# Kernel optimization log

Measured on AMD Instinct MI355X. Metric: run time of the kernel, lower is better.

Reference implementation:

```python
import jax, jax.numpy as jnp
import numpy as np

B, H, W, C = 8, 256, 256, 32
WIN = 8
HEADS = 2
DH = C // HEADS          # 16
HIDDEN = 128             # mlp_ratio * C
N = WIN * WIN            # 64 tokens per window


def _rel_index(win):
    # standard Swin relative position index, computed once (static int constant)
    coords = np.stack(np.meshgrid(np.arange(win), np.arange(win), indexing='ij'))  # [2,w,w]
    coords = coords.reshape(2, -1)                                                  # [2,N]
    rel = (coords[:, :, None] - coords[:, None, :]).transpose(1, 2, 0)              # [N,N,2]
    rel[:, :, 0] += win - 1
    rel[:, :, 1] += win - 1
    rel[:, :, 0] *= 2 * win - 1
    return jnp.asarray(rel.sum(-1))                                                 # [N,N]

REL_IDX = _rel_index(WIN)


def setup_inputs() -> dict:
    key = jax.random.key(0)
    ks = jax.random.split(key, 10)
    rn = lambda k, s: jax.random.normal(k, s, jnp.float32) * 0.02
    return {
        'x': jax.random.normal(ks[0], (B, H * W, C), jnp.float32),
        'norm1_g': jnp.ones((C,), jnp.float32), 'norm1_b': jnp.zeros((C,), jnp.float32),
        'wq': rn(ks[1], (C, C)), 'bq': jnp.zeros((C,), jnp.float32),
        'wkv': rn(ks[2], (C, 2 * C)), 'bkv': jnp.zeros((2 * C,), jnp.float32),
        'wo': rn(ks[3], (C, C)), 'bo': jnp.zeros((C,), jnp.float32),
        'rel_bias': rn(ks[4], ((2 * WIN - 1) ** 2, HEADS)),
        'norm2_g': jnp.ones((C,), jnp.float32), 'norm2_b': jnp.zeros((C,), jnp.float32),
        'w1': rn(ks[5], (C, HIDDEN)), 'b1': jnp.zeros((HIDDEN,), jnp.float32),
        'dw': rn(ks[6], (HIDDEN, 1, 3, 3)), 'dwb': jnp.zeros((HIDDEN,), jnp.float32),
        'w2': rn(ks[7], (HIDDEN, C)), 'b2': jnp.zeros((C,), jnp.float32),
    }


def _ln(x, g, b):
    mu = x.mean(-1, keepdims=True)
    var = x.var(-1, keepdims=True)
    return (x - mu) / jnp.sqrt(var + 1e-5) * g + b


def _gelu(x):
    return jax.nn.gelu(x, approximate=False)  # torch nn.GELU is exact erf


def reference(x, norm1_g, norm1_b, wq, bq, wkv, bkv, wo, bo, rel_bias,
              norm2_g, norm2_b, w1, b1, dw, dwb, w2, b2):
    shortcut = x                                              # [B, HW, C]
    xn = _ln(x, norm1_g, norm1_b).reshape(B, H, W, C)
    # window partition -> [B*nW, N, C]
    xw = (xn.reshape(B, H // WIN, WIN, W // WIN, WIN, C)
            .transpose(0, 1, 3, 2, 4, 5)
            .reshape(-1, N, C))
    # linear qkv projection
    q = (xw @ wq + bq).reshape(-1, N, HEADS, DH).transpose(0, 2, 1, 3)      # [B_,h,N,d]
    kv = (xw @ wkv + bkv).reshape(-1, N, 2, HEADS, DH).transpose(2, 0, 3, 1, 4)
    k, v = kv[0], kv[1]
    scale = DH ** -0.5
    attn = jnp.einsum('bhnd,bhmd->bhnm', q * scale, k)                      # [B_,h,N,N]
    bias = rel_bias[REL_IDX].transpose(2, 0, 1)                             # [h,N,N]
    attn = jax.nn.softmax(attn + bias[None], axis=-1)
    out = jnp.einsum('bhnm,bhmd->bhnd', attn, v).transpose(0, 2, 1, 3).reshape(-1, N, C)
    out = out @ wo + bo
    # window reverse -> [B, HW, C]
    out = (out.reshape(B, H // WIN, W // WIN, WIN, WIN, C)
              .transpose(0, 1, 3, 2, 4, 5)
              .reshape(B, H * W, C))
    x = shortcut + out
    # LeFF: linear -> dwconv3x3 over full HxW map -> linear
    y = _ln(x, norm2_g, norm2_b)
    y = _gelu(y @ w1 + b1)                                                  # [B,HW,HIDDEN]
    y = y.reshape(B, H, W, HIDDEN).transpose(0, 3, 1, 2)                    # NCHW
    y = jax.lax.conv_general_dilated(
        y, dw, window_strides=(1, 1), padding='SAME',
        dimension_numbers=('NCHW', 'OIHW', 'NCHW'), feature_group_count=HIDDEN)
    y = _gelu(y + dwb[None, :, None, None])
    y = y.transpose(0, 2, 3, 1).reshape(B, H * W, HIDDEN)
    y = y @ w2 + b2
    return x + y
```

## Files before the change

### kernel.cpp

```cpp
#include <hip/hip_runtime.h>
#include <hip/hip_bf16.h>
#include <math.h>

#define IMG   256
#define HWTOK 65536
#define CH    32

typedef __attribute__((ext_vector_type(8))) _Float16 half8v;
typedef __attribute__((ext_vector_type(2))) _Float16 half2v;
typedef __attribute__((ext_vector_type(4))) float floatx4;

__device__ __forceinline__ unsigned short f2h(float f) {
    _Float16 h = (_Float16)f;
    return __builtin_bit_cast(unsigned short, h);
}
__device__ __forceinline__ half2v pkrtz(float a, float b) {
    return __builtin_bit_cast(half2v, __builtin_amdgcn_cvt_pkrtz(a, b));
}
__device__ __forceinline__ unsigned packh2(float a, float b) {
    return __builtin_bit_cast(unsigned, __builtin_amdgcn_cvt_pkrtz(a, b));
}

__device__ __forceinline__ half2v gelu2v(half2v v) {
    const half2v hi = (half2v)(_Float16)( 2.0f);
    const half2v lo = (half2v)(_Float16)(-2.0f);
    const half2v vc = __builtin_elementwise_min(__builtin_elementwise_max(v, lo), hi);
    const half2v s  = vc * vc;
    half2v p = s * (half2v)(_Float16)(-1.18726e-3f) + (half2v)(_Float16)(9.97356e-3f);
    p = s * p + (half2v)(_Float16)(-6.64904e-2f);
    p = s * p + (half2v)(_Float16)( 3.989423e-1f);
    return v * (vc * p + (half2v)(_Float16)(0.5f));
}

__global__ __launch_bounds__(256) void prep_kernel(
    const float* __restrict__ w1, const float* __restrict__ w2,
    const float* __restrict__ wq, const float* __restrict__ wkv,
    const float* __restrict__ wo, const float* __restrict__ dw,
    const float* __restrict__ dwb, const float* __restrict__ relb,
    unsigned short* __restrict__ w1p, unsigned short* __restrict__ w2p,
    unsigned short* __restrict__ wqp, unsigned short* __restrict__ wkp,
    unsigned short* __restrict__ wvp, unsigned short* __restrict__ wop,
    unsigned short* __restrict__ dwp, unsigned short* __restrict__ dwbp,
    float* __restrict__ biasf)
{
    const float LOG2E = 1.4426950408889634f;
    const float QSC   = 0.25f * LOG2E;
    const int bid = blockIdx.x, tid = threadIdx.x;

    if (bid < 16) {
        const int t = bid * 256 + tid;
        const int row = t >> 5, k = t & 31;
        const int bl = row >> 5, wi = row & 31;
        const int j = bl * 32 + ((wi & 15) << 1) + (wi >> 4);
        w1p[t] = f2h(w1[k * 128 + j]);
        const int n = t >> 7, kk = t & 127;
        w2p[t] = f2h(w2[kk * 32 + n]);
    } else if (bid < 20) {
        const int u = (bid - 16) * 256 + tid;
        const int h = u >> 9, rem = u & 511;
        const int col = rem >> 5, k = rem & 31;
        wqp[u] = f2h(wq [k * 32 + h * 16 + col] * QSC);
        wkp[u] = f2h(wkv[k * 64 + h * 16 + col]);
        wvp[u] = f2h(wkv[k * 64 + 32 + h * 16 + col]);
        const int n = u >> 5, kk2 = u & 31;
        wop[u] = f2h(wo[kk2 * 32 + n]);
    } else if (bid < 28) {
        const int g = (bid - 20) * 256 + tid;
        const int h = g >> 10, nt = (g >> 8) & 3, mt = (g >> 6) & 3, l = g & 63;
        const int q = nt * 16 + (l & 15);
        const int mb = mt * 16 + (l >> 4) * 4;
        const int qy = q >> 3, qx = q & 7;
        #pragma unroll
        for (int r = 0; r < 4; ++r) {
            const int m = mb + r;
            const int my = m >> 3, mx = m & 7;
            const int idx = (qy - my + 7) * 15 + (qx - mx + 7);
            biasf[g * 4 + r] = relb[idx * 2 + h] * LOG2E;
        }
    } else {
        for (int e = tid; e < 1280; e += 256) {
            if (e < 1152) dwp[e] = f2h(dw[(e & 127) * 9 + (e >> 7)]);
            else          dwbp[e - 1152] = f2h(dwb[e - 1152]);
        }
    }
}

__global__ __launch_bounds__(128) void attn_kernel(
    const float* __restrict__ x,
    const float* __restrict__ n1g, const float* __restrict__ n1b,
    const float* __restrict__ bq,  const float* __restrict__ bkv,
    const float* __restrict__ bo,
    const unsigned short* __restrict__ wqp,
    const unsigned short* __restrict__ wkp,
    const unsigned short* __restrict__ wvp,
    const unsigned short* __restrict__ wop,
    const float4* __restrict__ biasf4,
    float* __restrict__ x1)
{
    struct Win {
        union {
            unsigned short xn[64][40];
            unsigned short P[2][64][72];
            unsigned short O[64][40];
        } u;
        unsigned short Q[64][40];
        unsigned short K[64][48];
        unsigned short VT[2][16][72];
    };
    __shared__ Win S;
    __shared__ float denom[2][64];

    const int tid = threadIdx.x;
    const int h   = tid >> 6;
    const int l   = tid & 63;
    const int lm  = l & 15, lq = l >> 4;

    const int win = blockIdx.x;
    const int b   = win >> 10;
    const int wh  = (win >> 5) & 31, ww = win & 31;
    const size_t wbase = ((size_t)b * HWTOK + (wh * 8) * IMG + ww * 8) * CH;

    const float LOG2E = 1.4426950408889634f;
    const float QSC   = 0.25f * LOG2E;

    const half8v bwq  = *(const half8v*)&wqp[h * 512 + lm * 32 + lq * 8];
    const half8v bwk  = *(const half8v*)&wkp[h * 512 + lm * 32 + lq * 8];
    const half8v bwv  = *(const half8v*)&wvp[h * 512 + lm * 32 + lq * 8];
    const half8v bwo0 = *(const half8v*)&wop[lm * 32 + lq * 8];
    const half8v bwo1 = *(const half8v*)&wop[(16 + lm) * 32 + lq * 8];

    {
        const int tok = tid >> 1, half = tid & 1;
        const size_t sbase = wbase
            + (size_t)((tok >> 3) * IMG + (tok & 7)) * CH + half * 16;
        const float4* xp = (const float4*)(x + sbase);
        float v[16];
        float s = 0.f;
        #pragma unroll
        for (int i = 0; i < 4; ++i) {
            const float4 t = xp[i];
            v[i*4+0]=t.x; v[i*4+1]=t.y; v[i*4+2]=t.z; v[i*4+3]=t.w;
            s += t.x + t.y + t.z + t.w;
        }
        const float mu = (s + __shfl_xor(s, 1)) * (1.f / 32.f);
        float qq = 0.f;
        #pragma unroll
        for (int c = 0; c < 16; ++c) { const float d = v[c] - mu; qq += d * d; }
        const float var = qq + __shfl_xor(qq, 1);
        const float inv = rsqrtf(var * (1.f / 32.f) + 1e-5f);
        unsigned pk[8];
        #pragma unroll
        for (int j = 0; j < 8; ++j) {
            const int c = half * 16 + 2 * j;
            pk[j] = packh2((v[2*j]   - mu) * inv * n1g[c]   + n1b[c],
                           (v[2*j+1] - mu) * inv * n1g[c+1] + n1b[c+1]);
        }
        uint4* dst = (uint4*)&S.u.xn[tok][half * 16];
        dst[0] = *(uint4*)&pk[0];
        dst[1] = *(uint4*)&pk[4];
        const uint4 z = {0u, 0u, 0u, 0u};
        *(uint4*)&S.K[tok][16 + half * 8] = z;
    }
    __syncthreads();

    const float bqv = bq[h*16 + lm] * QSC;
    const float bkv_ = bkv[h*16 + lm];
    const float bvv = bkv[32 + h*16 + lm];
    const floatx4 cq = {bqv, bqv, bqv, bqv};
    const floatx4 ck = {bkv_, bkv_, bkv_, bkv_};
    const floatx4 cv = {bvv, bvv, bvv, bvv};
    const floatx4 zero = {0.f, 0.f, 0.f, 0.f};

    #pragma unroll
    for (int mt = 0; mt < 4; ++mt) {
        const half8v a = *(const half8v*)&S.u.xn[mt*16 + lm][lq*8];
        const floatx4 dq = __builtin_amdgcn_mfma_f32_16x16x32_f16(a, bwq, cq, 0,0,0);
        const floatx4 dk = __builtin_amdgcn_mfma_f32_16x16x32_f16(a, bwk, ck, 0,0,0);
        const floatx4 dv = __builtin_amdgcn_mfma_f32_16x16x32_f16(a, bwv, cv, 0,0,0);
        const int r0 = mt*16 + lq*4;
        #pragma unroll
        for (int r = 0; r < 4; ++r) {
            S.Q[r0 + r][h*16 + lm] = f2h(dq[r]);
            S.K[r0 + r][h*32 + lm] = f2h(dk[r]);
        }
        uint2 vv;
        vv.x = packh2(dv[0], dv[1]);
        vv.y = packh2(dv[2], dv[3]);
        *(uint2*)&S.VT[h][lm][r0] = vv;
    }
    __syncthreads();

    half8v ak[4], bqf[4];
    #pragma unroll
    for (int mt = 0; mt < 4; ++mt)
        ak[mt] = *(const half8v*)&S.K[mt*16 + lm][h*16 + lq*8];
    #pragma unroll
    for (int nt = 0; nt < 4; ++nt)
        bqf[nt] = *(const half8v*)&S.Q[nt*16 + lm][lq*8];

    #pragma unroll
    for (int nt = 0; nt < 4; ++nt) {
        float sum = 0.f;
        #pragma unroll
        for (int mt = 0; mt < 4; ++mt) {
            const float4 cb = biasf4[(h*16 + nt*4 + mt) * 64 + l];
            const floatx4 C = {cb.x, cb.y, cb.z, cb.w};
            const floatx4 d = __builtin_amdgcn_mfma_f32_16x16x32_f16(ak[mt], bqf[nt], C, 0,0,0);
            const float e0 = exp2f(d[0]);
            const float e1 = exp2f(d[1]);
            const float e2 = exp2f(d[2]);
            const float e3 = exp2f(d[3]);
            sum += (e0 + e1) + (e2 + e3);
            uint2 pw;
            pw.x = packh2(e0, e1);
            pw.y = packh2(e2, e3);
            *(uint2*)&S.u.P[h][nt*16 + lm][mt*16 + lq*4] = pw;
        }
        sum += __shfl_xor(sum, 16);
        sum += __shfl_xor(sum, 32);
        if (l < 16) denom[h][nt*16 + l] = __frcp_rn(sum);
    }

    const half8v bva = *(const half8v*)&S.VT[h][lm][lq*8];
    const half8v bvb = *(const half8v*)&S.VT[h][lm][32 + lq*8];
    float oreg[16];
    #pragma unroll
    for (int mt = 0; mt < 4; ++mt) {
        const half8v ap0 = *(const half8v*)&S.u.P[h][mt*16 + lm][lq*8];
        const half8v ap1 = *(const half8v*)&S.u.P[h][mt*16 + lm][32 + lq*8];
        floatx4 ov = __builtin_amdgcn_mfma_f32_16x16x32_f16(ap0, bva, zero, 0,0,0);
        ov         = __builtin_amdgcn_mfma_f32_16x16x32_f16(ap1, bvb, ov,   0,0,0);
        const float4 dn = *(const float4*)&denom[h][mt*16 + lq*4];
        oreg[mt*4+0] = ov[0] * dn.x;
        oreg[mt*4+1] = ov[1] * dn.y;
        oreg[mt*4+2] = ov[2] * dn.z;
        oreg[mt*4+3] = ov[3] * dn.w;
    }
    __syncthreads();

    #pragma unroll
    for (int mt = 0; mt < 4; ++mt)
        #pragma unroll
        for (int r = 0; r < 4; ++r)
            S.u.O[mt*16 + lq*4 + r][h*16 + lm] = f2h(oreg[mt*4 + r]);
    __syncthreads();

    const float bo0 = bo[lm], bo1 = bo[16 + lm];
    const floatx4 co0 = {bo0, bo0, bo0, bo0};
    const floatx4 co1 = {bo1, bo1, bo1, bo1};
    #pragma unroll
    for (int mi = 0; mi < 2; ++mi) {
        const int mt = 2*h + mi;
        const half8v aO = *(const half8v*)&S.u.O[mt*16 + lm][lq*8];
        const floatx4 d0 = __builtin_amdgcn_mfma_f32_16x16x32_f16(aO, bwo0, co0, 0,0,0);
        const floatx4 d1 = __builtin_amdgcn_mfma_f32_16x16x32_f16(aO, bwo1, co1, 0,0,0);
        #pragma unroll
        for (int r = 0; r < 4; ++r) {
            const int t = mt*16 + lq*4 + r;
            const size_t g = wbase + (size_t)((t >> 3) * IMG + (t & 7)) * CH;
            x1[g + lm]      = x[g + lm]      + d0[r];
            x1[g + 16 + lm] = x[g + 16 + lm] + d1[r];
        }
    }
}

__global__ __launch_bounds__(256, 3) void leff_kernel_gw(
    const float* __restrict__ x1,
    const float* __restrict__ n2g, const float* __restrict__ n2b,
    const float* __restrict__ b1,  const float* __restrict__ b2,
    const unsigned short* __restrict__ w1p,
    const unsigned short* __restrict__ w2p,
    const unsigned short* __restrict__ dwp,
    const unsigned short* __restrict__ dwbp,
    float* __restrict__ out)
{
    __shared__ __align__(16) unsigned short xnA[112][40];
    union HG {
        unsigned short hid[100][128];
        unsigned short glA[64][132];
    };
    __shared__ __align__(16) HG hg;

    const int blk = blockIdx.x;
    const int b = blk >> 10, tyb = (blk >> 5) & 31, txb = blk & 31;
    const int y0 = tyb * 8, x0 = txb * 8;
    const int tid = threadIdx.x;
    const int wv = tid >> 6;
    const int l  = tid & 63;
    const int lm = l & 15;
    const int lq = l >> 4;
    const bool edge = (tyb == 0) | (tyb == 31) | (txb == 0) | (txb == 31);

    const half8v bf0 = *(const half8v*)&w1p[(wv * 32 + lm) * 32 + lq * 8];
    const half8v bf1 = *(const half8v*)&w1p[(wv * 32 + 16 + lm) * 32 + lq * 8];

    if (tid < 200) {
        const int px = tid >> 1, half = tid & 1;
        const int hy = px / 10, hx = px % 10;
        const int iy = y0 + hy - 1, ix = x0 + hx - 1;
        const bool inb = (iy >= 0 && iy < IMG && ix >= 0 && ix < IMG);
        unsigned int pk[8];
        if (inb) {
            const size_t base = ((size_t)b * HWTOK + iy * IMG + ix) * CH + half * 16;
            const float4* xp = (const float4*)(x1 + base);
            float v[16];
            float s = 0.f;
            #pragma unroll
            for (int i = 0; i < 4; ++i) {
                const float4 t = xp[i];
                v[i*4+0]=t.x; v[i*4+1]=t.y; v[i*4+2]=t.z; v[i*4+3]=t.w;
                s += t.x + t.y + t.z + t.w;
            }
            const float mu = (s + __shfl_xor(s, 1)) * (1.f / 32.f);
            float q = 0.f;
            #pragma unroll
            for (int c = 0; c < 16; ++c) { const float d = v[c]-mu; q += d*d; }
            const float var = q + __shfl_xor(q, 1);
            const float inv = rsqrtf(var * (1.f/32.f) + 1e-5f);
            #pragma unroll
            for (int j = 0; j < 8; ++j) {
                const int c = half*16 + 2*j;
                pk[j] = packh2((v[2*j]   - mu) * inv * n2g[c]   + n2b[c],
                               (v[2*j+1] - mu) * inv * n2g[c+1] + n2b[c+1]);
            }
        } else {
            #pragma unroll
            for (int j = 0; j < 8; ++j) pk[j] = 0u;
        }
        uint4* dst = (uint4*)&xnA[px][half * 16];
        dst[0] = *(uint4*)&pk[0];
        dst[1] = *(uint4*)&pk[4];
    } else if (tid < 248) {
        const int t2 = tid - 200;
        const uint4 z = {0u,0u,0u,0u};
        *(uint4*)&xnA[100 + (t2 >> 2)][(t2 & 3) * 8] = z;
    }
    __syncthreads();

    {
        const int c0 = wv * 32 + 2 * lm;
        const float bias0 = b1[c0], bias1 = b1[c0 + 1];
        const floatx4 cb0 = {bias0, bias0, bias0, bias0};
        const floatx4 cb1 = {bias1, bias1, bias1, bias1};
        for (int mt = 0; mt < 7; ++mt) {
            const half8v af = *(const half8v*)&xnA[mt * 16 + lm][lq * 8];
            floatx4 a0 = __builtin_amdgcn_mfma_f32_16x16x32_f16(af, bf0, cb0, 0, 0, 0);
            floatx4 a1 = __builtin_amdgcn_mfma_f32_16x16x32_f16(af, bf1, cb1, 0, 0, 0);
            #pragma unroll
            for (int r = 0; r < 4; ++r) {
                const int p = mt * 16 + lq * 4 + r;
                if (mt < 6 || p < 100) {
                    half2v g = gelu2v(pkrtz(a0[r], a1[r]));
                    unsigned int bits = __builtin_bit_cast(unsigned int, g);
                    if (edge) {
                        const int hy = (p * 205) >> 11;
                        const int hx = p - hy * 10;
                        const int iy = y0 + hy - 1, ix = x0 + hx - 1;
                        const bool inb = (iy >= 0) & (iy < IMG) & (ix >= 0) & (ix < IMG);
                        if (!inb) bits = 0u;
                    }
                    *(unsigned int*)&hg.hid[p][c0] = bits;
                }
            }
        }
    }
    __syncthreads();

    {
        const int jq = tid & 31, pg = tid >> 5;
        const int j0 = 4 * jq;
        half2v dwa[9], dwc[9];
        #pragma unroll
        for (int t = 0; t < 9; ++t) {
            const uint2 wp = *(const uint2*)&dwp[t * 128 + j0];
            dwa[t] = __builtin_bit_cast(half2v, wp.x);
            dwc[t] = __builtin_bit_cast(half2v, wp.y);
        }
        half2v acca[8], accc[8];
        {
            const uint2 bp = *(const uint2*)&dwbp[j0];
            const half2v dba = __builtin_bit_cast(half2v, bp.x);
            const half2v dbc = __builtin_bit_cast(half2v, bp.y);
            #pragma unroll
            for (int i = 0; i < 8; ++i) { acca[i] = dba; accc[i] = dbc; }
        }
        #pragma unroll
        for (int ky = 0; ky < 3; ++ky) {
            uint2 rr[10];
            #pragma unroll
            for (int cx = 0; cx < 10; ++cx)
                rr[cx] = *(const uint2*)&hg.hid[(pg + ky) * 10 + cx][j0];
            #pragma unroll
            for (int i = 0; i < 8; ++i)
                #pragma unroll
                for (int kx = 0; kx < 3; ++kx) {
                    acca[i] = __builtin_bit_cast(half2v, rr[i + kx].x) * dwa[ky*3+kx] + acca[i];
                    accc[i] = __builtin_bit_cast(half2v, rr[i + kx].y) * dwc[ky*3+kx] + accc[i];
                }
        }
        __syncthreads();
        #pragma unroll
        for (int i = 0; i < 8; ++i) {
            const half2v ga = gelu2v(acca[i]);
            const half2v gc = gelu2v(accc[i]);
            uint2 ow;
            ow.x = __builtin_bit_cast(unsigned int, ga);
            ow.y = __builtin_bit_cast(unsigned int, gc);
            *(uint2*)&hg.glA[pg * 8 + i][j0] = ow;
        }
    }
    __syncthreads();

    {
        half8v w2f[2][4];
        #pragma unroll
        for (int nt = 0; nt < 2; ++nt)
            #pragma unroll
            for (int kc = 0; kc < 4; ++kc)
                w2f[nt][kc] = *(const half8v*)&w2p[(nt*16 + lm) * 128 + kc*32 + lq*8];
        #pragma unroll
        for (int nt = 0; nt < 2; ++nt) {
            const int mt = wv;
            const int c = nt * 16 + lm;
            const float bias = b2[c];
            floatx4 acc = {bias, bias, bias, bias};
            #pragma unroll
            for (int kc = 0; kc < 4; ++kc) {
                const half8v a = *(const half8v*)&hg.glA[mt * 16 + lm][kc * 32 + lq * 8];
                acc = __builtin_amdgcn_mfma_f32_16x16x32_f16(a, w2f[nt][kc], acc, 0, 0, 0);
            }
            #pragma unroll
            for (int r = 0; r < 4; ++r) {
                const int p = mt * 16 + lq * 4 + r;
                const int iy = y0 + (p >> 3), ix = x0 + (p & 7);
                const size_t g = ((size_t)b * HWTOK + iy * IMG + ix) * CH + c;
                out[g] = x1[g] + acc[r];
            }
        }
    }
}

extern "C" void kernel_launch(void* const* d_in, const int* in_sizes, int n_in,
                              void* d_out, int out_size, void* d_ws, size_t ws_size,
                              hipStream_t stream)
{
    const float* x    = (const float*)d_in[0];
    const float* n1g  = (const float*)d_in[1];
    const float* n1b  = (const float*)d_in[2];
    const float* wq   = (const float*)d_in[3];
    const float* bq   = (const float*)d_in[4];
    const float* wkv  = (const float*)d_in[5];
    const float* bkv  = (const float*)d_in[6];
    const float* wo   = (const float*)d_in[7];
    const float* bo   = (const float*)d_in[8];
    const float* relb = (const float*)d_in[9];
    const float* n2g  = (const float*)d_in[10];
    const float* n2b  = (const float*)d_in[11];
    const float* w1   = (const float*)d_in[12];
    const float* b1   = (const float*)d_in[13];
    const float* dw   = (const float*)d_in[14];
    const float* dwb  = (const float*)d_in[15];
    const float* w2   = (const float*)d_in[16];
    const float* b2   = (const float*)d_in[17];

    float* out = (float*)d_out;
    float* x1  = (float*)d_ws;
    char* base = (char*)d_ws + (size_t)8 * HWTOK * CH * 4;
    unsigned short* w1p  = (unsigned short*)(base);
    unsigned short* w2p  = (unsigned short*)(base + 8192);
    unsigned short* wqp  = (unsigned short*)(base + 16384);
    unsigned short* wkp  = (unsigned short*)(base + 18432);
    unsigned short* wvp  = (unsigned short*)(base + 20480);
    unsigned short* wop  = (unsigned short*)(base + 22528);
    unsigned short* dwp  = (unsigned short*)(base + 24576);
    unsigned short* dwbp = (unsigned short*)(base + 26880);
    float*          bias = (float*)(base + 28672);

    prep_kernel<<<29, 256, 0, stream>>>(w1, w2, wq, wkv, wo, dw, dwb, relb,
                                        w1p, w2p, wqp, wkp, wvp, wop,
                                        dwp, dwbp, bias);
    attn_kernel<<<8192, 128, 0, stream>>>(x, n1g, n1b, bq, bkv, bo,
                                          wqp, wkp, wvp, wop,
                                          (const float4*)bias, x1);
    leff_kernel_gw<<<8192, 256, 0, stream>>>(x1, n2g, n2b, b1, b2,
                                             w1p, w2p, dwp, dwbp, out);
}
```

Baseline: 140.3 us.

## Double threads per window in attention and LeFF kernels, splitting work across waves

Both kernels now launch twice as many threads per block: attention uses 4 waves (2 heads × 2 row-halves) and LeFF uses 8 waves, with LayerNorm loads split four ways per token, MFMA row tiles split between waves, and the depthwise conv handling 2 channels per thread instead of 4. The aim is more parallelism and latency hiding per window with less serial work per wave. In exchange there are more threads, more shuffles, and higher occupancy demands. A leftover dead loop in attention LN writes pk before it is overwritten.

```diff
diff --git a/kernel.cpp b/kernel.cpp
--- a/kernel.cpp
+++ b/kernel.cpp
@@ -85,7 +85,7 @@
     }
 }
 
-__global__ __launch_bounds__(128) void attn_kernel(
+__global__ __launch_bounds__(256, 3) void attn_kernel(
     const float* __restrict__ x,
     const float* __restrict__ n1g, const float* __restrict__ n1b,
     const float* __restrict__ bq,  const float* __restrict__ bkv,
@@ -111,7 +111,9 @@
     __shared__ float denom[2][64];
 
     const int tid = threadIdx.x;
-    const int h   = tid >> 6;
+    const int wv  = tid >> 6;
+    const int h   = wv & 1;
+    const int s2  = wv >> 1;
     const int l   = tid & 63;
     const int lm  = l & 15, lq = l >> 4;
 
@@ -130,36 +132,44 @@
     const half8v bwo1 = *(const half8v*)&wop[(16 + lm) * 32 + lq * 8];
 
     {
-        const int tok = tid >> 1, half = tid & 1;
+        const int tok = tid >> 2, q4 = tid & 3;
         const size_t sbase = wbase
-            + (size_t)((tok >> 3) * IMG + (tok & 7)) * CH + half * 16;
+            + (size_t)((tok >> 3) * IMG + (tok & 7)) * CH + q4 * 8;
         const float4* xp = (const float4*)(x + sbase);
-        float v[16];
+        float v[8];
         float s = 0.f;
         #pragma unroll
-        for (int i = 0; i < 4; ++i) {
+        for (int i = 0; i < 2; ++i) {
             const float4 t = xp[i];
             v[i*4+0]=t.x; v[i*4+1]=t.y; v[i*4+2]=t.z; v[i*4+3]=t.w;
             s += t.x + t.y + t.z + t.w;
         }
-        const float mu = (s + __shfl_xor(s, 1)) * (1.f / 32.f);
+        s += __shfl_xor(s, 1);
+        s += __shfl_xor(s, 2);
+        const float mu = s * (1.f / 32.f);
         float qq = 0.f;
         #pragma unroll
-        for (int c = 0; c < 16; ++c) { const float d = v[c] - mu; qq += d * d; }
-        const float var = qq + __shfl_xor(qq, 1);
-        const float inv = rsqrtf(var * (1.f / 32.f) + 1e-5f);
-        unsigned pk[8];
-        #pragma unroll
-        for (int j = 0; j < 8; ++j) {
-            const int c = half * 16 + 2 * j;
+        for (int c = 0; c < 8; ++c) { const float d = v[c] - mu; qq += d * d; }
+        qq += __shfl_xor(qq, 1);
+        qq += __shfl_xor(qq, 2);
+        const float inv = rsqrtf(qq * (1.f / 32.f) + 1e-5f);
+        unsigned pk[4];
+        #pragma unroll
+        for (int j = 0; j < 4; ++j) {
+            const int c = q4 * 8 + 2 * j;
+            pk[j] = packh2(v[2*j]   * inv - mu * inv * 1.f, 0.f);
+        }
+        #pragma unroll
+        for (int j = 0; j < 4; ++j) {
+            const int c = q4 * 8 + 2 * j;
             pk[j] = packh2((v[2*j]   - mu) * inv * n1g[c]   + n1b[c],
                            (v[2*j+1] - mu) * inv * n1g[c+1] + n1b[c+1]);
         }
-        uint4* dst = (uint4*)&S.u.xn[tok][half * 16];
-        dst[0] = *(uint4*)&pk[0];
-        dst[1] = *(uint4*)&pk[4];
-        const uint4 z = {0u, 0u, 0u, 0u};
-        *(uint4*)&S.K[tok][16 + half * 8] = z;
+        *(uint4*)&S.u.xn[tok][q4 * 8] = *(uint4*)&pk[0];
+        if (q4 < 2) {
+            const uint4 z = {0u, 0u, 0u, 0u};
+            *(uint4*)&S.K[tok][16 + q4 * 8] = z;
+        }
     }
     __syncthreads();
 
@@ -172,7 +182,8 @@
     const floatx4 zero = {0.f, 0.f, 0.f, 0.f};
 
     #pragma unroll
-    for (int mt = 0; mt < 4; ++mt) {
+    for (int mi = 0; mi < 2; ++mi) {
+        const int mt = 2*s2 + mi;
         const half8v a = *(const half8v*)&S.u.xn[mt*16 + lm][lq*8];
         const floatx4 dq = __builtin_amdgcn_mfma_f32_16x16x32_f16(a, bwq, cq, 0,0,0);
         const floatx4 dk = __builtin_amdgcn_mfma_f32_16x16x32_f16(a, bwk, ck, 0,0,0);
@@ -190,22 +201,21 @@
     }
     __syncthreads();
 
-    half8v ak[4], bqf[4];
+    half8v ak[4];
     #pragma unroll
     for (int mt = 0; mt < 4; ++mt)
         ak[mt] = *(const half8v*)&S.K[mt*16 + lm][h*16 + lq*8];
+
     #pragma unroll
-    for (int nt = 0; nt < 4; ++nt)
-        bqf[nt] = *(const half8v*)&S.Q[nt*16 + lm][lq*8];
-
-    #pragma unroll
-    for (int nt = 0; nt < 4; ++nt) {
+    for (int ni = 0; ni < 2; ++ni) {
+        const int nt = 2*s2 + ni;
+        const half8v bq_ = *(const half8v*)&S.Q[nt*16 + lm][lq*8];
         float sum = 0.f;
         #pragma unroll
         for (int mt = 0; mt < 4; ++mt) {
             const float4 cb = biasf4[(h*16 + nt*4 + mt) * 64 + l];
             const floatx4 C = {cb.x, cb.y, cb.z, cb.w};
-            const floatx4 d = __builtin_amdgcn_mfma_f32_16x16x32_f16(ak[mt], bqf[nt], C, 0,0,0);
+            const floatx4 d = __builtin_amdgcn_mfma_f32_16x16x32_f16(ak[mt], bq_, C, 0,0,0);
             const float e0 = exp2f(d[0]);
             const float e1 = exp2f(d[1]);
             const float e2 = exp2f(d[2]);
@@ -223,34 +233,36 @@
 
     const half8v bva = *(const half8v*)&S.VT[h][lm][lq*8];
     const half8v bvb = *(const half8v*)&S.VT[h][lm][32 + lq*8];
-    float oreg[16];
+    float oreg[8];
     #pragma unroll
-    for (int mt = 0; mt < 4; ++mt) {
+    for (int mi = 0; mi < 2; ++mi) {
+        const int mt = 2*s2 + mi;
         const half8v ap0 = *(const half8v*)&S.u.P[h][mt*16 + lm][lq*8];
         const half8v ap1 = *(const half8v*)&S.u.P[h][mt*16 + lm][32 + lq*8];
         floatx4 ov = __builtin_amdgcn_mfma_f32_16x16x32_f16(ap0, bva, zero, 0,0,0);
         ov         = __builtin_amdgcn_mfma_f32_16x16x32_f16(ap1, bvb, ov,   0,0,0);
         const float4 dn = *(const float4*)&denom[h][mt*16 + lq*4];
-        oreg[mt*4+0] = ov[0] * dn.x;
-        oreg[mt*4+1] = ov[1] * dn.y;
-        oreg[mt*4+2] = ov[2] * dn.z;
-        oreg[mt*4+3] = ov[3] * dn.w;
-    }
-    __syncthreads();
-
-    #pragma unroll
-    for (int mt = 0; mt < 4; ++mt)
-        #pragma unroll
-        for (int r = 0; r < 4; ++r)
-            S.u.O[mt*16 + lq*4 + r][h*16 + lm] = f2h(oreg[mt*4 + r]);
-    __syncthreads();
-
-    const float bo0 = bo[lm], bo1 = bo[16 + lm];
-    const floatx4 co0 = {bo0, bo0, bo0, bo0};
-    const floatx4 co1 = {bo1, bo1, bo1, bo1};
+        oreg[mi*4+0] = ov[0] * dn.x;
+        oreg[mi*4+1] = ov[1] * dn.y;
+        oreg[mi*4+2] = ov[2] * dn.z;
+        oreg[mi*4+3] = ov[3] * dn.w;
+    }
+    __syncthreads();
+
     #pragma unroll
     for (int mi = 0; mi < 2; ++mi) {
-        const int mt = 2*h + mi;
+        const int mt = 2*s2 + mi;
+        #pragma unroll
+        for (int r = 0; r < 4; ++r)
+            S.u.O[mt*16 + lq*4 + r][h*16 + lm] = f2h(oreg[mi*4 + r]);
+    }
+    __syncthreads();
+
+    {
+        const int mt = wv;
+        const float bo0 = bo[lm], bo1 = bo[16 + lm];
+        const floatx4 co0 = {bo0, bo0, bo0, bo0};
+        const floatx4 co1 = {bo1, bo1, bo1, bo1};
         const half8v aO = *(const half8v*)&S.u.O[mt*16 + lm][lq*8];
         const floatx4 d0 = __builtin_amdgcn_mfma_f32_16x16x32_f16(aO, bwo0, co0, 0,0,0);
         const floatx4 d1 = __builtin_amdgcn_mfma_f32_16x16x32_f16(aO, bwo1, co1, 0,0,0);
@@ -264,7 +276,7 @@
     }
 }
 
-__global__ __launch_bounds__(256, 3) void leff_kernel_gw(
+__global__ __launch_bounds__(512, 6) void leff_kernel_gw(
     const float* __restrict__ x1,
     const float* __restrict__ n2g, const float* __restrict__ n2b,
     const float* __restrict__ b1,  const float* __restrict__ b2,
@@ -291,58 +303,62 @@
     const int lq = l >> 4;
     const bool edge = (tyb == 0) | (tyb == 31) | (txb == 0) | (txb == 31);
 
-    const half8v bf0 = *(const half8v*)&w1p[(wv * 32 + lm) * 32 + lq * 8];
-    const half8v bf1 = *(const half8v*)&w1p[(wv * 32 + 16 + lm) * 32 + lq * 8];
-
-    if (tid < 200) {
-        const int px = tid >> 1, half = tid & 1;
+    const int cb = wv >> 1, mhalf = wv & 1;
+    const half8v bf0 = *(const half8v*)&w1p[(cb * 32 + lm) * 32 + lq * 8];
+    const half8v bf1 = *(const half8v*)&w1p[(cb * 32 + 16 + lm) * 32 + lq * 8];
+
+    if (tid < 400) {
+        const int px = tid >> 2, q4 = tid & 3;
         const int hy = px / 10, hx = px % 10;
         const int iy = y0 + hy - 1, ix = x0 + hx - 1;
         const bool inb = (iy >= 0 && iy < IMG && ix >= 0 && ix < IMG);
-        unsigned int pk[8];
+        unsigned pk[4];
         if (inb) {
-            const size_t base = ((size_t)b * HWTOK + iy * IMG + ix) * CH + half * 16;
+            const size_t base = ((size_t)b * HWTOK + iy * IMG + ix) * CH + q4 * 8;
             const float4* xp = (const float4*)(x1 + base);
-            float v[16];
+            float v[8];
             float s = 0.f;
             #pragma unroll
-            for (int i = 0; i < 4; ++i) {
+            for (int i = 0; i < 2; ++i) {
                 const float4 t = xp[i];
                 v[i*4+0]=t.x; v[i*4+1]=t.y; v[i*4+2]=t.z; v[i*4+3]=t.w;
                 s += t.x + t.y + t.z + t.w;
             }
-            const float mu = (s + __shfl_xor(s, 1)) * (1.f / 32.f);
-            float q = 0.f;
-            #pragma unroll
-            for (int c = 0; c < 16; ++c) { const float d = v[c]-mu; q += d*d; }
-            const float var = q + __shfl_xor(q, 1);
-            const float inv = rsqrtf(var * (1.f/32.f) + 1e-5f);
-            #pragma unroll
-            for (int j = 0; j < 8; ++j) {
-                const int c = half*16 + 2*j;
+            s += __shfl_xor(s, 1);
+            s += __shfl_xor(s, 2);
+            const float mu = s * (1.f / 32.f);
+            float qq = 0.f;
+            #pragma unroll
+            for (int c = 0; c < 8; ++c) { const float d = v[c]-mu; qq += d*d; }
+            qq += __shfl_xor(qq, 1);
+            qq += __shfl_xor(qq, 2);
+            const float inv = rsqrtf(qq * (1.f/32.f) + 1e-5f);
+            #pragma unroll
+            for (int j = 0; j < 4; ++j) {
+                const int c = q4 * 8 + 2 * j;
                 pk[j] = packh2((v[2*j]   - mu) * inv * n2g[c]   + n2b[c],
                                (v[2*j+1] - mu) * inv * n2g[c+1] + n2b[c+1]);
             }
         } else {
             #pragma unroll
-            for (int j = 0; j < 8; ++j) pk[j] = 0u;
-        }
-        uint4* dst = (uint4*)&xnA[px][half * 16];
-        dst[0] = *(uint4*)&pk[0];
-        dst[1] = *(uint4*)&pk[4];
-    } else if (tid < 248) {
-        const int t2 = tid - 200;
+            for (int j = 0; j < 4; ++j) pk[j] = 0u;
+        }
+        *(uint4*)&xnA[px][q4 * 8] = *(uint4*)&pk[0];
+    } else if (tid < 448) {
+        const int t2 = tid - 400;
         const uint4 z = {0u,0u,0u,0u};
         *(uint4*)&xnA[100 + (t2 >> 2)][(t2 & 3) * 8] = z;
     }
     __syncthreads();
 
     {
-        const int c0 = wv * 32 + 2 * lm;
+        const int c0 = cb * 32 + 2 * lm;
         const float bias0 = b1[c0], bias1 = b1[c0 + 1];
         const floatx4 cb0 = {bias0, bias0, bias0, bias0};
         const floatx4 cb1 = {bias1, bias1, bias1, bias1};
-        for (int mt = 0; mt < 7; ++mt) {
+        const int mt0 = mhalf ? 4 : 0;
+        const int mtN = mhalf ? 7 : 4;
+        for (int mt = mt0; mt < mtN; ++mt) {
             const half8v af = *(const half8v*)&xnA[mt * 16 + lm][lq * 8];
             floatx4 a0 = __builtin_amdgcn_mfma_f32_16x16x32_f16(af, bf0, cb0, 0, 0, 0);
             floatx4 a1 = __builtin_amdgcn_mfma_f32_16x16x32_f16(af, bf1, cb1, 0, 0, 0);
@@ -367,75 +383,59 @@
     __syncthreads();
 
     {
-        const int jq = tid & 31, pg = tid >> 5;
-        const int j0 = 4 * jq;
-        half2v dwa[9], dwc[9];
-        #pragma unroll
-        for (int t = 0; t < 9; ++t) {
-            const uint2 wp = *(const uint2*)&dwp[t * 128 + j0];
-            dwa[t] = __builtin_bit_cast(half2v, wp.x);
-            dwc[t] = __builtin_bit_cast(half2v, wp.y);
-        }
-        half2v acca[8], accc[8];
+        const int jq = tid & 63, pg = tid >> 6;
+        const int j0 = 2 * jq;
+        half2v dwa[9];
+        #pragma unroll
+        for (int t = 0; t < 9; ++t)
+            dwa[t] = __builtin_bit_cast(half2v, *(const unsigned*)&dwp[t * 128 + j0]);
+        half2v acc[8];
         {
-            const uint2 bp = *(const uint2*)&dwbp[j0];
-            const half2v dba = __builtin_bit_cast(half2v, bp.x);
-            const half2v dbc = __builtin_bit_cast(half2v, bp.y);
-            #pragma unroll
-            for (int i = 0; i < 8; ++i) { acca[i] = dba; accc[i] = dbc; }
+            const half2v dba = __builtin_bit_cast(half2v, *(const unsigned*)&dwbp[j0]);
+            #pragma unroll
+            for (int i = 0; i < 8; ++i) acc[i] = dba;
         }
         #pragma unroll
         for (int ky = 0; ky < 3; ++ky) {
-            uint2 rr[10];
+            unsigned rr[10];
             #pragma unroll
             for (int cx = 0; cx < 10; ++cx)
-                rr[cx] = *(const uint2*)&hg.hid[(pg + ky) * 10 + cx][j0];
+                rr[cx] = *(const unsigned*)&hg.hid[(pg + ky) * 10 + cx][j0];
             #pragma unroll
             for (int i = 0; i < 8; ++i)
                 #pragma unroll
-                for (int kx = 0; kx < 3; ++kx) {
-                    acca[i] = __builtin_bit_cast(half2v, rr[i + kx].x) * dwa[ky*3+kx] + acca[i];
-                    accc[i] = __builtin_bit_cast(half2v, rr[i + kx].y) * dwc[ky*3+kx] + accc[i];
-                }
+                for (int kx = 0; kx < 3; ++kx)
+                    acc[i] = __builtin_bit_cast(half2v, rr[i + kx]) * dwa[ky*3+kx] + acc[i];
         }
         __syncthreads();
         #pragma unroll
         for (int i = 0; i < 8; ++i) {
-            const half2v ga = gelu2v(acca[i]);
-            const half2v gc = gelu2v(accc[i]);
-            uint2 ow;
-            ow.x = __builtin_bit_cast(unsigned int, ga);
-            ow.y = __builtin_bit_cast(unsigned int, gc);
-            *(uint2*)&hg.glA[pg * 8 + i][j0] = ow;
+            const half2v g = gelu2v(acc[i]);
+            *(unsigned*)&hg.glA[pg * 8 + i][j0] = __builtin_bit_cast(unsigned, g);
         }
     }
     __syncthreads();
 
     {
-        half8v w2f[2][4];
-        #pragma unroll
-        for (int nt = 0; nt < 2; ++nt)
-            #pragma unroll
-            for (int kc = 0; kc < 4; ++kc)
-                w2f[nt][kc] = *(const half8v*)&w2p[(nt*16 + lm) * 128 + kc*32 + lq*8];
-        #pragma unroll
-        for (int nt = 0; nt < 2; ++nt) {
-            const int mt = wv;
-            const int c = nt * 16 + lm;
-            const float bias = b2[c];
-            floatx4 acc = {bias, bias, bias, bias};
-            #pragma unroll
-            for (int kc = 0; kc < 4; ++kc) {
-                const half8v a = *(const half8v*)&hg.glA[mt * 16 + lm][kc * 32 + lq * 8];
-                acc = __builtin_amdgcn_mfma_f32_16x16x32_f16(a, w2f[nt][kc], acc, 0, 0, 0);
-            }
-            #pragma unroll
-            for (int r = 0; r < 4; ++r) {
-                const int p = mt * 16 + lq * 4 + r;
-                const int iy = y0 + (p >> 3), ix = x0 + (p & 7);
-                const size_t g = ((size_t)b * HWTOK + iy * IMG + ix) * CH + c;
-                out[g] = x1[g] + acc[r];
-            }
+        const int mt = wv >> 1, nt = wv & 1;
+        half8v w2f[4];
+        #pragma unroll
+        for (int kc = 0; kc < 4; ++kc)
+            w2f[kc] = *(const half8v*)&w2p[(nt*16 + lm) * 128 + kc*32 + lq*8];
+        const int c = nt * 16 + lm;
+        const float bias = b2[c];
+        floatx4 acc = {bias, bias, bias, bias};
+        #pragma unroll
+        for (int kc = 0; kc < 4; ++kc) {
+            const half8v a = *(const half8v*)&hg.glA[mt * 16 + lm][kc * 32 + lq * 8];
+            acc = __builtin_amdgcn_mfma_f32_16x16x32_f16(a, w2f[kc], acc, 0, 0, 0);
+        }
+        #pragma unroll
+        for (int r = 0; r < 4; ++r) {
+            const int p = mt * 16 + lq * 4 + r;
+            const int iy = y0 + (p >> 3), ix = x0 + (p & 7);
+            const size_t g = ((size_t)b * HWTOK + iy * IMG + ix) * CH + c;
+            out[g] = x1[g] + acc[r];
         }
     }
 }
@@ -479,9 +479,9 @@
     prep_kernel<<<29, 256, 0, stream>>>(w1, w2, wq, wkv, wo, dw, dwb, relb,
                                         w1p, w2p, wqp, wkp, wvp, wop,
                                         dwp, dwbp, bias);
-    attn_kernel<<<8192, 128, 0, stream>>>(x, n1g, n1b, bq, bkv, bo,
+    attn_kernel<<<8192, 256, 0, stream>>>(x, n1g, n1b, bq, bkv, bo,
                                           wqp, wkp, wvp, wop,
                                           (const float4*)bias, x1);
-    leff_kernel_gw<<<8192, 256, 0, stream>>>(x1, n2g, n2b, b1, b2,
+    leff_kernel_gw<<<8192, 512, 0, stream>>>(x1, n2g, n2b, b1, b2,
                                              w1p, w2p, dwp, dwbp, out);
 }
```

Measured after the change: 131.2 us. 1.07x faster.
